# Optimization experiments

Hardware: AMD Instinct MI355X
Metric: run time of the kernel (lower is better)

Reference implementation:

```python
import jax, jax.numpy as jnp
import numpy as np

B, S, D, H = 2, 2048, 1024, 16
HD = D // H
SCALE_FACTOR = 0.2  # ScalableSoftmax scale


def setup_inputs() -> dict:
    key = jax.random.key(0)
    ks = jax.random.split(key, 5)
    inv = 1.0 / np.sqrt(D)
    return {
        "x": jax.random.normal(ks[0], (B, S, D), dtype=jnp.float32),
        "qkv_w": jax.random.normal(ks[1], (3 * D, D), dtype=jnp.float32) * inv,
        "qkv_b": jax.random.normal(ks[2], (3 * D,), dtype=jnp.float32) * 0.02,
        "out_w": jax.random.normal(ks[3], (D, D), dtype=jnp.float32) * inv,
        "out_b": jax.random.normal(ks[4], (D,), dtype=jnp.float32) * 0.02,
    }


def reference(x, qkv_w, qkv_b, out_w, out_b):
    b, s, d = x.shape
    # qkv projection: [b, s, 3d] -> [b, h, s, 3*hd]
    qkv = (jnp.einsum("bsd,ed->bse", x, qkv_w) + qkv_b)
    qkv = qkv.reshape(b, s, H, 3 * HD).transpose(0, 2, 1, 3)
    q, k, v = jnp.split(qkv, 3, axis=-1)  # each [b, h, s, hd]
    # scaled dot-product scores, then ScalableSoftmax: softmax(0.2 * scores)
    scores = jnp.einsum("bhqd,bhkd->bhqk", q, k) / jnp.sqrt(jnp.float32(HD))
    attn = jax.nn.softmax(SCALE_FACTOR * scores, axis=-1)
    vals = jnp.einsum("bhqk,bhkd->bhqd", attn, v)
    vals = vals.transpose(0, 2, 1, 3).reshape(b, s, d)
    return jnp.einsum("bsd,ed->bse", vals, out_w) + out_b
```

## Files before the change

### kernel.cpp

```cpp
#include <hip/hip_runtime.h>

using bh8    = __attribute__((ext_vector_type(8)))  short;
using f32x4v = __attribute__((ext_vector_type(4)))  float;
using f32x16 = __attribute__((ext_vector_type(16))) float;
using u32x4  = __attribute__((ext_vector_type(4)))  unsigned int;
using us4    = __attribute__((ext_vector_type(4)))  unsigned short;

#define AS1 __attribute__((address_space(1)))
#define AS3 __attribute__((address_space(3)))

#define B_  2
#define S_  2048
#define D_  1024
#define H_  16
#define HD_ 64
#define C2A 0.0360673760222241f

__device__ __forceinline__ unsigned short f2bf(float f) {
  unsigned u = __builtin_bit_cast(unsigned, f);
  return (unsigned short)((u + 0x7fffu + ((u >> 16) & 1u)) >> 16);
}
__device__ __forceinline__ int swz8(int r) { return (r ^ (r >> 3)) & 7; }

__global__ __launch_bounds__(256) void cvt_all(const float* __restrict__ x,
                                               const float* __restrict__ qw,
                                               const float* __restrict__ ow,
                                               unsigned short* __restrict__ xb,
                                               unsigned short* __restrict__ qwb,
                                               unsigned short* __restrict__ owb) {
  int i = blockIdx.x * 256 + threadIdx.x;
  const float* src; unsigned short* dst; int off;
  if (i < 1048576)      { src = x;  dst = xb;  off = i; }
  else if (i < 1835008) { src = qw; dst = qwb; off = i - 1048576; }
  else                  { src = ow; dst = owb; off = i - 1835008; }
  f32x4v v = reinterpret_cast<const f32x4v*>(src)[off];
  us4 o;
  o[0] = f2bf(v[0]); o[1] = f2bf(v[1]); o[2] = f2bf(v[2]); o[3] = f2bf(v[3]);
  reinterpret_cast<us4*>(dst)[off] = o;
}

template <int MODE>
__global__ __launch_bounds__(256) void gemm_bt(const unsigned short* __restrict__ A,
                                               const unsigned short* __restrict__ Bw,
                                               const float* __restrict__ bias,
                                               float* __restrict__ Cf,
                                               unsigned short* __restrict__ Qo,
                                               unsigned short* __restrict__ Ko,
                                               unsigned short* __restrict__ Vo,
                                               int M, int N, int K) {
  __shared__ __align__(16) short As[128 * 64];
  __shared__ __align__(16) short Bs[128 * 64];
  const int tid = threadIdx.x;
  const int w = tid >> 6, l = tid & 63;
  const int lr = l & 15, lg = l >> 4;
  const int m0 = blockIdx.x * 128, n0 = blockIdx.y * 128;
  const int wm = (w >> 1) * 64, wn = (w & 1) * 64;

  f32x4v acc[4][4];
#pragma unroll
  for (int a = 0; a < 4; a++)
#pragma unroll
    for (int b = 0; b < 4; b++)
#pragma unroll
      for (int r = 0; r < 4; r++) acc[a][b][r] = 0.f;

#pragma unroll 1
  for (int k0 = 0; k0 < K; k0 += 64) {
    __syncthreads();
#pragma unroll
    for (int n = 0; n < 4; n++) {
      int idx = n * 256 + tid;
      int row = idx >> 3, p = idx & 7;
      int c = p ^ swz8(row);
      const unsigned short* srcA = A + (size_t)(m0 + row) * K + k0 + c * 8;
      const unsigned short* srcB = Bw + (size_t)(n0 + row) * K + k0 + c * 8;
      __builtin_amdgcn_global_load_lds((const AS1 void*)srcA,
          (AS3 void*)((char*)As + (n * 256 + w * 64) * 16), 16, 0, 0);
      __builtin_amdgcn_global_load_lds((const AS1 void*)srcB,
          (AS3 void*)((char*)Bs + (n * 256 + w * 64) * 16), 16, 0, 0);
    }
    __syncthreads();
#pragma unroll
    for (int kk = 0; kk < 2; kk++) {
      bh8 af[4], bf[4];
#pragma unroll
      for (int mi = 0; mi < 4; mi++) {
        int row = wm + mi * 16 + lr;
        int slot = (4 * kk + lg) ^ swz8(row);
        af[mi] = *(const bh8*)((const char*)As + row * 128 + slot * 16);
      }
#pragma unroll
      for (int ni = 0; ni < 4; ni++) {
        int row = wn + ni * 16 + lr;
        int slot = (4 * kk + lg) ^ swz8(row);
        bf[ni] = *(const bh8*)((const char*)Bs + row * 128 + slot * 16);
      }
#pragma unroll
      for (int mi = 0; mi < 4; mi++)
#pragma unroll
        for (int ni = 0; ni < 4; ni++)
          acc[mi][ni] = __builtin_amdgcn_mfma_f32_16x16x32_bf16(af[mi], bf[ni], acc[mi][ni], 0, 0, 0);
    }
  }

  if (MODE == 1) {
#pragma unroll
    for (int ni = 0; ni < 4; ni++) {
      int e = n0 + wn + ni * 16 + lr;
      float bv = bias[e];
#pragma unroll
      for (int mi = 0; mi < 4; mi++) {
        int mbase = m0 + wm + mi * 16 + lg * 4;
#pragma unroll
        for (int r = 0; r < 4; r++)
          Cf[(size_t)(mbase + r) * N + e] = acc[mi][ni][r] + bv;
      }
    }
  } else {
#pragma unroll
    for (int ni = 0; ni < 4; ni++) {
      int e = n0 + wn + ni * 16 + lr;
      int hh = e / 192;
      int rr = e - hh * 192;
      int tsel = rr >> 6, d = rr & 63;
      float bv = bias[e];
#pragma unroll
      for (int mi = 0; mi < 4; mi++) {
        int mbase = m0 + wm + mi * 16 + lg * 4;
#pragma unroll
        for (int r = 0; r < 4; r++) {
          int m = mbase + r;
          int b = m >> 11, s = m & 2047;
          float val = acc[mi][ni][r] + bv;
          size_t bh = (size_t)(b * H_ + hh);
          if (tsel == 0)      Qo[(bh * S_ + s) * HD_ + d] = f2bf(val * C2A);
          else if (tsel == 1) Ko[(bh * S_ + s) * HD_ + d] = f2bf(val);
          else                Vo[(bh * HD_ + d) * S_ + s] = f2bf(val);
        }
      }
    }
  }
}

__global__ __launch_bounds__(256) void attn_fwd(const unsigned short* __restrict__ Qt,
                                                const unsigned short* __restrict__ Kt,
                                                const unsigned short* __restrict__ VT,
                                                unsigned short* __restrict__ vals) {
  __shared__ __align__(16) short Ks[2 * 64 * 64];
  __shared__ __align__(16) short Vs[2 * 64 * 64];
  const int tid = threadIdx.x, w = tid >> 6, l = tid & 63;
  const int lq = l & 31, h = l >> 5;
  const int lin = blockIdx.x;
  const int uu_ = lin >> 3;
  const int bh = (lin & 7) + 8 * (uu_ & 3);
  const int q0 = (uu_ >> 2) * 128 + w * 32;
  const unsigned short* Qp = Qt + (size_t)bh * (S_ * HD_);
  const unsigned short* Kp = Kt + (size_t)bh * (S_ * HD_);
  const unsigned short* Vp = VT + (size_t)bh * (HD_ * S_);

  bh8 qf[4];
#pragma unroll
  for (int kf = 0; kf < 4; kf++)
    qf[kf] = *(const bh8*)(Qp + (size_t)(q0 + lq) * HD_ + kf * 16 + h * 8);

  f32x16 KZ;
#pragma unroll
  for (int r = 0; r < 16; r++) KZ[r] = 0.f;
  bh8 ones;
#pragma unroll
  for (int j = 0; j < 8; j++) ones[j] = (short)0x3F80;

  f32x16 O[2], Ol;
  O[0] = KZ; O[1] = KZ; Ol = KZ;

  const int row0 = tid >> 3,        c0 = (tid & 7) ^ swz8(row0);
  const int row1 = (256 + tid) >> 3, c1 = (tid & 7) ^ swz8(row1);
  const unsigned short* kp0 = Kp + row0 * HD_ + c0 * 8;
  const unsigned short* kp1 = Kp + row1 * HD_ + c1 * 8;
  const unsigned short* vp0 = Vp + (size_t)row0 * S_ + c0 * 8;
  const unsigned short* vp1 = Vp + (size_t)row1 * S_ + c1 * 8;
  char* dK = (char*)Ks + w * 64 * 16;
  char* dV = (char*)Vs + w * 64 * 16;

  auto stage = [&](int t, int buf) {
    __builtin_amdgcn_global_load_lds((const AS1 void*)(kp0 + (size_t)t * 4096),
                                     (AS3 void*)(dK + buf * 8192), 16, 0, 0);
    __builtin_amdgcn_global_load_lds((const AS1 void*)(kp1 + (size_t)t * 4096),
                                     (AS3 void*)(dK + buf * 8192 + 4096), 16, 0, 0);
    __builtin_amdgcn_global_load_lds((const AS1 void*)(vp0 + (size_t)t * 64),
                                     (AS3 void*)(dV + buf * 8192), 16, 0, 0);
    __builtin_amdgcn_global_load_lds((const AS1 void*)(vp1 + (size_t)t * 64),
                                     (AS3 void*)(dV + buf * 8192 + 4096), 16, 0, 0);
  };

  int ko0[4], ko1[4], vo0[4], vo1[4];
#pragma unroll
  for (int kf = 0; kf < 4; kf++) {
    int r0 = lq, r1 = 32 + lq;
    ko0[kf] = r0 * 128 + (((2 * kf + h) ^ swz8(r0)) << 4);
    ko1[kf] = r1 * 128 + (((2 * kf + h) ^ swz8(r1)) << 4);
  }
#pragma unroll
  for (int c = 0; c < 2; c++)
#pragma unroll
    for (int ni = 0; ni < 2; ni++) {
      int d = ni * 32 + lq;
      vo0[c * 2 + ni] = d * 128 + (((2 * c + h) ^ swz8(d)) << 4);
      vo1[c * 2 + ni] = d * 128 + (((4 + 2 * c + h) ^ swz8(d)) << 4);
    }

  stage(0, 0);
#pragma unroll 1
  for (int i = 0; i < 32; i++) {
    const int cur = i & 1;
    asm volatile("s_waitcnt vmcnt(0)" ::: "memory");
    __builtin_amdgcn_s_barrier();
    if (i < 31) stage(i + 1, cur ^ 1);
    const char* Kc = (const char*)Ks + cur * 8192;
    const char* Vc = (const char*)Vs + cur * 8192;

    f32x16 sa, sb;
    __builtin_amdgcn_s_setprio(1);
    {
      bh8 k0 = *(const bh8*)(Kc + ko0[0]);
      bh8 k1 = *(const bh8*)(Kc + ko1[0]);
      sa = __builtin_amdgcn_mfma_f32_32x32x16_bf16(k0, qf[0], KZ, 0, 0, 0);
      sb = __builtin_amdgcn_mfma_f32_32x32x16_bf16(k1, qf[0], KZ, 0, 0, 0);
    }
#pragma unroll
    for (int kf = 1; kf < 4; kf++) {
      bh8 k0 = *(const bh8*)(Kc + ko0[kf]);
      bh8 k1 = *(const bh8*)(Kc + ko1[kf]);
      sa = __builtin_amdgcn_mfma_f32_32x32x16_bf16(k0, qf[kf], sa, 0, 0, 0);
      sb = __builtin_amdgcn_mfma_f32_32x32x16_bf16(k1, qf[kf], sb, 0, 0, 0);
    }
    __builtin_amdgcn_s_setprio(0);

    float pa_[16], pb_[16];
#pragma unroll
    for (int r = 0; r < 16; r++)
      asm("v_exp_f32 %0, %1" : "=v"(pa_[r]) : "v"(sa[r]));
    unsigned wa0[4], wa1[4];
#pragma unroll
    for (int g = 0; g < 4; g++) {
      asm("v_cvt_pk_bf16_f32 %0, %1, %2" : "=v"(wa0[g]) : "v"(pa_[4 * g]), "v"(pa_[4 * g + 1]));
      asm("v_cvt_pk_bf16_f32 %0, %1, %2" : "=v"(wa1[g]) : "v"(pa_[4 * g + 2]), "v"(pa_[4 * g + 3]));
    }
#pragma unroll
    for (int r = 0; r < 16; r++)
      asm("v_exp_f32 %0, %1" : "=v"(pb_[r]) : "v"(sb[r]));
    unsigned wb0[4], wb1[4];
#pragma unroll
    for (int g = 0; g < 4; g++) {
      asm("v_cvt_pk_bf16_f32 %0, %1, %2" : "=v"(wb0[g]) : "v"(pb_[4 * g]), "v"(pb_[4 * g + 1]));
      asm("v_cvt_pk_bf16_f32 %0, %1, %2" : "=v"(wb1[g]) : "v"(pb_[4 * g + 2]), "v"(pb_[4 * g + 3]));
    }

    bh8 paf[2], pbf[2];
#pragma unroll
    for (int c = 0; c < 2; c++) {
      unsigned x0 = wa0[2 * c], y0 = wa0[2 * c + 1];
      unsigned x1 = wa1[2 * c], y1 = wa1[2 * c + 1];
      asm("v_permlane32_swap_b32 %0, %1" : "+v"(x0), "+v"(y0));
      asm("v_permlane32_swap_b32 %0, %1" : "+v"(x1), "+v"(y1));
      u32x4 up; up[0] = x0; up[1] = x1; up[2] = y0; up[3] = y1;
      paf[c] = __builtin_bit_cast(bh8, up);
    }
#pragma unroll
    for (int c = 0; c < 2; c++) {
      unsigned x0 = wb0[2 * c], y0 = wb0[2 * c + 1];
      unsigned x1 = wb1[2 * c], y1 = wb1[2 * c + 1];
      asm("v_permlane32_swap_b32 %0, %1" : "+v"(x0), "+v"(y0));
      asm("v_permlane32_swap_b32 %0, %1" : "+v"(x1), "+v"(y1));
      u32x4 up; up[0] = x0; up[1] = x1; up[2] = y0; up[3] = y1;
      pbf[c] = __builtin_bit_cast(bh8, up);
    }

    __builtin_amdgcn_s_setprio(1);
#pragma unroll
    for (int c = 0; c < 2; c++) {
      bh8 vf0 = *(const bh8*)(Vc + vo0[c * 2 + 0]);
      bh8 vf1 = *(const bh8*)(Vc + vo0[c * 2 + 1]);
      O[0] = __builtin_amdgcn_mfma_f32_32x32x16_bf16(paf[c], vf0, O[0], 0, 0, 0);
      O[1] = __builtin_amdgcn_mfma_f32_32x32x16_bf16(paf[c], vf1, O[1], 0, 0, 0);
      Ol   = __builtin_amdgcn_mfma_f32_32x32x16_bf16(paf[c], ones, Ol, 0, 0, 0);
    }
#pragma unroll
    for (int c = 0; c < 2; c++) {
      bh8 vf0 = *(const bh8*)(Vc + vo1[c * 2 + 0]);
      bh8 vf1 = *(const bh8*)(Vc + vo1[c * 2 + 1]);
      O[0] = __builtin_amdgcn_mfma_f32_32x32x16_bf16(pbf[c], vf0, O[0], 0, 0, 0);
      O[1] = __builtin_amdgcn_mfma_f32_32x32x16_bf16(pbf[c], vf1, O[1], 0, 0, 0);
      Ol   = __builtin_amdgcn_mfma_f32_32x32x16_bf16(pbf[c], ones, Ol, 0, 0, 0);
    }
    __builtin_amdgcn_s_setprio(0);
  }

  float rl[16];
#pragma unroll
  for (int r = 0; r < 16; r++) rl[r] = __builtin_amdgcn_rcpf(Ol[r]);

  const int b = bh >> 4, hh = bh & 15;
#pragma unroll
  for (int ni = 0; ni < 2; ni++) {
    int d = ni * 32 + lq;
#pragma unroll
    for (int r = 0; r < 16; r++) {
      float vvv = O[ni][r] * rl[r];
      int qg = q0 + 4 * h + 8 * (r >> 2) + (r & 3);
      vals[((size_t)(b * S_ + qg)) * D_ + hh * HD_ + d] = f2bf(vvv);
    }
  }
}

extern "C" void kernel_launch(void* const* d_in, const int* in_sizes, int n_in,
                              void* d_out, int out_size, void* d_ws, size_t ws_size,
                              hipStream_t stream) {
  const float* x     = (const float*)d_in[0];
  const float* qkv_w = (const float*)d_in[1];
  const float* qkv_b = (const float*)d_in[2];
  const float* out_w = (const float*)d_in[3];
  const float* out_b = (const float*)d_in[4];
  float* out = (float*)d_out;

  unsigned short* xb  = (unsigned short*)d_ws;
  unsigned short* qwb = xb  + (size_t)4096 * 1024;
  unsigned short* owb = qwb + (size_t)3072 * 1024;
  unsigned short* Qb  = owb + (size_t)1024 * 1024;
  unsigned short* Kb  = Qb  + (size_t)32 * 2048 * 64;
  unsigned short* Vb  = Kb  + (size_t)32 * 2048 * 64;
  unsigned short* vb  = Vb  + (size_t)32 * 2048 * 64;

  cvt_all<<<8192, 256, 0, stream>>>(x, qkv_w, out_w, xb, qwb, owb);
  gemm_bt<0><<<dim3(32, 24), 256, 0, stream>>>(xb, qwb, qkv_b, nullptr, Qb, Kb, Vb,
                                               4096, 3072, 1024);
  attn_fwd<<<512, 256, 0, stream>>>(Qb, Kb, Vb, vb);
  gemm_bt<1><<<dim3(32, 8), 256, 0, stream>>>(vb, owb, out_b, out, nullptr, nullptr, nullptr,
                                              4096, 1024, 1024);
}
```

Baseline: 120.2 us.

## Widen attention blocks to 8 waves and use 64-row tiles for out-projection

The attention kernel now runs 512-thread blocks covering 256 queries. Eight waves share one K/V tile in LDS, so each thread issues a single staging load per tile instead of two, and K/V global traffic per query is halved. The output-projection GEMM is templated to a 64x128 tile with each wave owning a 32-column slice, which doubles the grid to 512 blocks for better CU fill. In exchange, attention has fewer, larger blocks that may be harder to schedule, and the smaller GEMM tile reuses each B tile across fewer rows.

New measurement: 116.9 us. 2.7% less time.

```diff
diff --git a/kernel.cpp b/kernel.cpp
--- a/kernel.cpp
+++ b/kernel.cpp
@@ -39,7 +39,7 @@
   reinterpret_cast<us4*>(dst)[off] = o;
 }
 
-template <int MODE>
+template <int MODE, int BM>
 __global__ __launch_bounds__(256) void gemm_bt(const unsigned short* __restrict__ A,
                                                const unsigned short* __restrict__ Bw,
                                                const float* __restrict__ bias,
@@ -48,41 +48,50 @@
                                                unsigned short* __restrict__ Ko,
                                                unsigned short* __restrict__ Vo,
                                                int M, int N, int K) {
-  __shared__ __align__(16) short As[128 * 64];
+  constexpr int NIW = (BM == 128) ? 4 : 2;
+  constexpr int NA  = BM / 32;
+  __shared__ __align__(16) short As[BM * 64];
   __shared__ __align__(16) short Bs[128 * 64];
   const int tid = threadIdx.x;
   const int w = tid >> 6, l = tid & 63;
   const int lr = l & 15, lg = l >> 4;
-  const int m0 = blockIdx.x * 128, n0 = blockIdx.y * 128;
-  const int wm = (w >> 1) * 64, wn = (w & 1) * 64;
-
-  f32x4v acc[4][4];
+  const int m0 = blockIdx.x * BM, n0 = blockIdx.y * 128;
+  const int wm = (BM == 128) ? (w >> 1) * 64 : 0;
+  const int wn = (BM == 128) ? (w & 1) * 64 : w * 32;
+
+  f32x4v acc[4][NIW];
 #pragma unroll
   for (int a = 0; a < 4; a++)
 #pragma unroll
-    for (int b = 0; b < 4; b++)
+    for (int b = 0; b < NIW; b++)
 #pragma unroll
       for (int r = 0; r < 4; r++) acc[a][b][r] = 0.f;
 
 #pragma unroll 1
   for (int k0 = 0; k0 < K; k0 += 64) {
     __syncthreads();
+#pragma unroll
+    for (int n = 0; n < NA; n++) {
+      int idx = n * 256 + tid;
+      int row = idx >> 3, p = idx & 7;
+      int c = p ^ swz8(row);
+      const unsigned short* srcA = A + (size_t)(m0 + row) * K + k0 + c * 8;
+      __builtin_amdgcn_global_load_lds((const AS1 void*)srcA,
+          (AS3 void*)((char*)As + (n * 256 + w * 64) * 16), 16, 0, 0);
+    }
 #pragma unroll
     for (int n = 0; n < 4; n++) {
       int idx = n * 256 + tid;
       int row = idx >> 3, p = idx & 7;
       int c = p ^ swz8(row);
-      const unsigned short* srcA = A + (size_t)(m0 + row) * K + k0 + c * 8;
       const unsigned short* srcB = Bw + (size_t)(n0 + row) * K + k0 + c * 8;
-      __builtin_amdgcn_global_load_lds((const AS1 void*)srcA,
-          (AS3 void*)((char*)As + (n * 256 + w * 64) * 16), 16, 0, 0);
       __builtin_amdgcn_global_load_lds((const AS1 void*)srcB,
           (AS3 void*)((char*)Bs + (n * 256 + w * 64) * 16), 16, 0, 0);
     }
     __syncthreads();
 #pragma unroll
     for (int kk = 0; kk < 2; kk++) {
-      bh8 af[4], bf[4];
+      bh8 af[4], bf[NIW];
 #pragma unroll
       for (int mi = 0; mi < 4; mi++) {
         int row = wm + mi * 16 + lr;
@@ -90,7 +99,7 @@
         af[mi] = *(const bh8*)((const char*)As + row * 128 + slot * 16);
       }
 #pragma unroll
-      for (int ni = 0; ni < 4; ni++) {
+      for (int ni = 0; ni < NIW; ni++) {
         int row = wn + ni * 16 + lr;
         int slot = (4 * kk + lg) ^ swz8(row);
         bf[ni] = *(const bh8*)((const char*)Bs + row * 128 + slot * 16);
@@ -98,14 +107,14 @@
 #pragma unroll
       for (int mi = 0; mi < 4; mi++)
 #pragma unroll
-        for (int ni = 0; ni < 4; ni++)
+        for (int ni = 0; ni < NIW; ni++)
           acc[mi][ni] = __builtin_amdgcn_mfma_f32_16x16x32_bf16(af[mi], bf[ni], acc[mi][ni], 0, 0, 0);
     }
   }
 
   if (MODE == 1) {
 #pragma unroll
-    for (int ni = 0; ni < 4; ni++) {
+    for (int ni = 0; ni < NIW; ni++) {
       int e = n0 + wn + ni * 16 + lr;
       float bv = bias[e];
 #pragma unroll
@@ -118,7 +127,7 @@
     }
   } else {
 #pragma unroll
-    for (int ni = 0; ni < 4; ni++) {
+    for (int ni = 0; ni < NIW; ni++) {
       int e = n0 + wn + ni * 16 + lr;
       int hh = e / 192;
       int rr = e - hh * 192;
@@ -142,7 +151,7 @@
   }
 }
 
-__global__ __launch_bounds__(256) void attn_fwd(const unsigned short* __restrict__ Qt,
+__global__ __launch_bounds__(512) void attn_fwd(const unsigned short* __restrict__ Qt,
                                                 const unsigned short* __restrict__ Kt,
                                                 const unsigned short* __restrict__ VT,
                                                 unsigned short* __restrict__ vals) {
@@ -153,7 +162,7 @@
   const int lin = blockIdx.x;
   const int uu_ = lin >> 3;
   const int bh = (lin & 7) + 8 * (uu_ & 3);
-  const int q0 = (uu_ >> 2) * 128 + w * 32;
+  const int q0 = (uu_ >> 2) * 256 + w * 32;
   const unsigned short* Qp = Qt + (size_t)bh * (S_ * HD_);
   const unsigned short* Kp = Kt + (size_t)bh * (S_ * HD_);
   const unsigned short* Vp = VT + (size_t)bh * (HD_ * S_);
@@ -173,24 +182,17 @@
   f32x16 O[2], Ol;
   O[0] = KZ; O[1] = KZ; Ol = KZ;
 
-  const int row0 = tid >> 3,        c0 = (tid & 7) ^ swz8(row0);
-  const int row1 = (256 + tid) >> 3, c1 = (tid & 7) ^ swz8(row1);
-  const unsigned short* kp0 = Kp + row0 * HD_ + c0 * 8;
-  const unsigned short* kp1 = Kp + row1 * HD_ + c1 * 8;
-  const unsigned short* vp0 = Vp + (size_t)row0 * S_ + c0 * 8;
-  const unsigned short* vp1 = Vp + (size_t)row1 * S_ + c1 * 8;
-  char* dK = (char*)Ks + w * 64 * 16;
-  char* dV = (char*)Vs + w * 64 * 16;
+  const int row0 = tid >> 3, cc = (tid & 7) ^ swz8(row0);
+  const unsigned short* kp0 = Kp + row0 * HD_ + cc * 8;
+  const unsigned short* vp0 = Vp + (size_t)row0 * S_ + cc * 8;
+  char* dK = (char*)Ks + w * 1024;
+  char* dV = (char*)Vs + w * 1024;
 
   auto stage = [&](int t, int buf) {
     __builtin_amdgcn_global_load_lds((const AS1 void*)(kp0 + (size_t)t * 4096),
                                      (AS3 void*)(dK + buf * 8192), 16, 0, 0);
-    __builtin_amdgcn_global_load_lds((const AS1 void*)(kp1 + (size_t)t * 4096),
-                                     (AS3 void*)(dK + buf * 8192 + 4096), 16, 0, 0);
     __builtin_amdgcn_global_load_lds((const AS1 void*)(vp0 + (size_t)t * 64),
                                      (AS3 void*)(dV + buf * 8192), 16, 0, 0);
-    __builtin_amdgcn_global_load_lds((const AS1 void*)(vp1 + (size_t)t * 64),
-                                     (AS3 void*)(dV + buf * 8192 + 4096), 16, 0, 0);
   };
 
   int ko0[4], ko1[4], vo0[4], vo1[4];
@@ -332,9 +334,9 @@
   unsigned short* vb  = Vb  + (size_t)32 * 2048 * 64;
 
   cvt_all<<<8192, 256, 0, stream>>>(x, qkv_w, out_w, xb, qwb, owb);
-  gemm_bt<0><<<dim3(32, 24), 256, 0, stream>>>(xb, qwb, qkv_b, nullptr, Qb, Kb, Vb,
-                                               4096, 3072, 1024);
-  attn_fwd<<<512, 256, 0, stream>>>(Qb, Kb, Vb, vb);
-  gemm_bt<1><<<dim3(32, 8), 256, 0, stream>>>(vb, owb, out_b, out, nullptr, nullptr, nullptr,
-                                              4096, 1024, 1024);
-}
+  gemm_bt<0, 128><<<dim3(32, 24), 256, 0, stream>>>(xb, qwb, qkv_b, nullptr, Qb, Kb, Vb,
+                                                    4096, 3072, 1024);
+  attn_fwd<<<256, 512, 0, stream>>>(Qb, Kb, Vb, vb);
+  gemm_bt<1, 64><<<dim3(64, 8), 256, 0, stream>>>(vb, owb, out_b, out, nullptr, nullptr, nullptr,
+                                                  4096, 1024, 1024);
+}
```
